# Kernel tuning notes

Measured on AMD Instinct MI355X. Metric: run time of the kernel, lower is better.

The kernel has to match this reference:

```python
import jax, jax.numpy as jnp
import numpy as np

B, S, D, H, E, K = 4, 512, 512, 2048, 8, 2
LN_EPS = 1e-5

def _ln(x, g, b):
    m = jnp.mean(x, axis=-1, keepdims=True)
    v = jnp.var(x, axis=-1, keepdims=True)
    return (x - m) / jnp.sqrt(v + LN_EPS) * g + b

def setup_inputs() -> dict:
    key = jax.random.key(0)
    ks = jax.random.split(key, 8)
    s = 0.02
    return {
        "x": jax.random.normal(ks[0], (B, S, D), dtype=jnp.float32),
        "context": jax.random.normal(ks[1], (B, S, D), dtype=jnp.float32),
        "quality": jax.random.uniform(ks[2], (B, 1), dtype=jnp.float32),
        "rn_g": jnp.ones((D,), jnp.float32), "rn_b": jnp.zeros((D,), jnp.float32),
        "cn_g": jnp.ones((D,), jnp.float32), "cn_b": jnp.zeros((D,), jnp.float32),
        "ctx_W": jax.random.normal(ks[3], (D, D), dtype=jnp.float32) * s,
        "ctx_b": jnp.zeros((D,), jnp.float32),
        "qual_W": jax.random.normal(ks[4], (1, D), dtype=jnp.float32) * s,
        "qual_b": jnp.zeros((D,), jnp.float32),
        "rtr_W": jax.random.normal(ks[5], (D, E), dtype=jnp.float32) * s,
        "rtr_b": jnp.zeros((E,), jnp.float32),
        "temperature": jnp.asarray(1.0, jnp.float32),
        "W1": jax.random.normal(ks[6], (E, D, H), dtype=jnp.float32) * s,
        "b1": jnp.zeros((E, H), jnp.float32),
        "W2": jax.random.normal(ks[7], (E, H, D), dtype=jnp.float32) * s,
        "b2": jnp.zeros((E, D), jnp.float32),
    }

def reference(x, context, quality, rn_g, rn_b, cn_g, cn_b, ctx_W, ctx_b,
              qual_W, qual_b, rtr_W, rtr_b, temperature, W1, b1, W2, b2):
    # router features: LN(x) + context_proj(LN(context)) + quality_proj(quality)
    rf = _ln(x, rn_g, rn_b) + (_ln(context, cn_g, cn_b) @ ctx_W + ctx_b)
    q = quality[:, None, :]                      # [B,1,1]
    rf = rf + (q @ qual_W + qual_b)              # broadcast [B,1,D] over seq
    logits = (rf @ rtr_W + rtr_b) / jnp.maximum(temperature, 0.25)  # [B,S,E]
    # eval mode: no router noise, no dropout
    topk_logits, topk_idx = jax.lax.top_k(logits, K)
    gates = jax.nn.softmax(topk_logits, axis=-1)                    # [B,S,K]
    # per-token per-expert combine weight (equivalent to masked dispatch)
    combine = jnp.sum(gates[..., None] * jax.nn.one_hot(topk_idx, E, dtype=x.dtype), axis=-2)  # [B,S,E]
    # dense all-expert FFN, combined with (mostly zero) gate weights
    h = jax.nn.gelu(jnp.einsum('bsd,edh->bseh', x, W1) + b1, approximate=False)  # [B,S,E,H]
    y = jnp.einsum('bseh,ehd->bsed', h, W2) + b2                                 # [B,S,E,D]
    out = jnp.einsum('bsed,bse->bsd', y, combine)
    # aux losses
    probs = jax.nn.softmax(logits, axis=-1)
    importance = probs.mean(axis=(0, 1))
    load_balance = jnp.mean((importance - 1.0 / E) ** 2)
    router_z = jnp.mean(jax.scipy.special.logsumexp(logits, axis=-1) ** 2)
    entropy = jnp.mean(-jnp.sum(probs * jnp.log(jnp.clip(probs, 1e-9, None)), axis=-1))
    aux = load_balance + 1e-3 * router_z - 1e-3 * entropy
    return out, load_balance, router_z, entropy, aux
```

## Files before the change

### kernel.cpp

```cpp
#include <hip/hip_runtime.h>
#include <hip/hip_bf16.h>
#include <math.h>

#define Bb 4
#define Ss 512
#define Dd 512
#define Hh 2048
#define Ee 8
#define TOKENS 2048
#define CAP 2048

typedef __attribute__((ext_vector_type(8))) _Float16 f16x8;
typedef __attribute__((ext_vector_type(4))) _Float16 f16x4;
typedef __attribute__((ext_vector_type(4))) float f32x4;

#define WS_CNT   0
#define WS_OFFS  32
#define WS_M1    128
#define WS_QV    16512
#define WS_CB    16544
#define WS_LIST  16640
#define WS_GLIST 82176
#define WS_LOG   147712
#define WS_XF    (WS_LOG + 65536)
#define WS_W1F   (WS_XF + 2097152)
#define WS_W2F   (WS_W1F + 16777216)
#define WS_HF    (WS_W2F + 16777216)

__device__ __forceinline__ float wred(float v) {
#pragma unroll
  for (int o = 32; o > 0; o >>= 1) v += __shfl_down(v, o);
  return v;
}

__device__ __forceinline__ float wredx(float v) {
#pragma unroll
  for (int o = 32; o > 0; o >>= 1) v += __shfl_xor(v, o);
  return v;
}

__device__ __forceinline__ float block_sum(float v, float* s4, int tid) {
  v = wred(v);
  __syncthreads();
  if ((tid & 63) == 0) s4[tid >> 6] = v;
  __syncthreads();
  return s4[0] + s4[1] + s4[2] + s4[3];
}

__device__ __forceinline__ float gelu_f(float v) {
  return 0.5f * v * (1.0f + erff(v * 0.7071067811865475f));
}

#define GL16(gp, lp) __builtin_amdgcn_global_load_lds( \
    (const __attribute__((address_space(1))) void*)(gp), \
    (__attribute__((address_space(3))) void*)(lp), 16, 0, 0)

__device__ __forceinline__ void convT_tile(const float* __restrict__ src,
    _Float16* __restrict__ dst, int R, int C, int bx, float* ls) {
  int nr = R >> 6, ncc = C >> 6;
  int e = bx / (nr * ncc);
  int rem = bx % (nr * ncc);
  int rt = rem / ncc, ct = rem % ncc;
  int tid = threadIdx.x;
  const float* s0 = src + (size_t)e * R * C + (size_t)(rt * 64) * C + ct * 64;
#pragma unroll
  for (int j = 0; j < 4; j++) {
    int li = j * 256 + tid;
    int rr = li >> 4, c4 = (li & 15) << 2;
    float4 v = *(const float4*)(s0 + (size_t)rr * C + c4);
    ls[rr * 65 + c4] = v.x;
    ls[rr * 65 + c4 + 1] = v.y;
    ls[rr * 65 + c4 + 2] = v.z;
    ls[rr * 65 + c4 + 3] = v.w;
  }
  __syncthreads();
#pragma unroll
  for (int j = 0; j < 4; j++) {
    int li = j * 256 + tid;
    int on = li >> 4, k4 = (li & 15) << 2;
    f16x4 o;
    o[0] = (_Float16)ls[(k4 + 0) * 65 + on];
    o[1] = (_Float16)ls[(k4 + 1) * 65 + on];
    o[2] = (_Float16)ls[(k4 + 2) * 65 + on];
    o[3] = (_Float16)ls[(k4 + 3) * 65 + on];
    *(f16x4*)(dst + ((size_t)e * C + ct * 64 + on) * R + rt * 64 + k4) = o;
  }
}

__global__ __launch_bounds__(256) void k_pre(
    const float* __restrict__ ctx_W, const float* __restrict__ rtr_W,
    const float* __restrict__ rtr_b, const float* __restrict__ qual_W,
    const float* __restrict__ qual_b, const float* __restrict__ ctx_b,
    const float* __restrict__ W1, const float* __restrict__ W2,
    float* __restrict__ M1, float* __restrict__ qv, float* __restrict__ cb,
    _Float16* __restrict__ w1f, _Float16* __restrict__ w2f) {
  __shared__ float ls[64 * 65];
  int bx = blockIdx.x;
  if (bx >= 513) {
    int cx = bx - 513;
    if (cx < Ee * 8 * 32) convT_tile(W1, w1f, Dd, Hh, cx, ls);
    else convT_tile(W2, w2f, Hh, Dd, cx - Ee * 8 * 32, ls);
    return;
  }
  int d = bx;
  int tid = threadIdx.x;
  if (tid >= 64) return;
  int lane = tid;
  if (d < Dd) {
    float acc[Ee] = {0.f, 0.f, 0.f, 0.f, 0.f, 0.f, 0.f, 0.f};
    for (int k = lane; k < Dd; k += 64) {
      float cw = ctx_W[d * Dd + k];
      const float* r = rtr_W + k * Ee;
#pragma unroll
      for (int e = 0; e < Ee; e++) acc[e] += cw * r[e];
    }
#pragma unroll
    for (int e = 0; e < Ee; e++) acc[e] = wred(acc[e]);
    if (lane == 0) {
#pragma unroll
      for (int e = 0; e < Ee; e++) M1[d * Ee + e] = acc[e];
    }
  } else {
    float aq[Ee] = {0.f, 0.f, 0.f, 0.f, 0.f, 0.f, 0.f, 0.f};
    float ab[Ee] = {0.f, 0.f, 0.f, 0.f, 0.f, 0.f, 0.f, 0.f};
    for (int k = lane; k < Dd; k += 64) {
      float qw = qual_W[k];
      float bb = ctx_b[k] + qual_b[k];
      const float* r = rtr_W + k * Ee;
#pragma unroll
      for (int e = 0; e < Ee; e++) {
        aq[e] += qw * r[e];
        ab[e] += bb * r[e];
      }
    }
#pragma unroll
    for (int e = 0; e < Ee; e++) {
      aq[e] = wred(aq[e]);
      ab[e] = wred(ab[e]);
    }
    if (lane == 0) {
#pragma unroll
      for (int e = 0; e < Ee; e++) {
        qv[e] = aq[e];
        cb[e] = ab[e] + rtr_b[e];
      }
    }
  }
}

__global__ __launch_bounds__(256) void k_logits(
    const float* __restrict__ x, const float* __restrict__ ctx,
    const float* __restrict__ quality, const float* __restrict__ rn_g,
    const float* __restrict__ rn_b, const float* __restrict__ cn_g,
    const float* __restrict__ cn_b, const float* __restrict__ rtr_W,
    const float* __restrict__ M1, const float* __restrict__ qv,
    const float* __restrict__ cb, const float* __restrict__ temperature,
    float* __restrict__ logitsS, _Float16* __restrict__ xf) {
  int wid = threadIdx.x >> 6, lane = threadIdx.x & 63;
  int t = blockIdx.x * 4 + wid;
  int d0 = lane * 8;

  float xv[8], cv[8];
  *(float4*)&xv[0] = *(const float4*)(x + (size_t)t * Dd + d0);
  *(float4*)&xv[4] = *(const float4*)(x + (size_t)t * Dd + d0 + 4);
  *(float4*)&cv[0] = *(const float4*)(ctx + (size_t)t * Dd + d0);
  *(float4*)&cv[4] = *(const float4*)(ctx + (size_t)t * Dd + d0 + 4);

  f16x8 xh;
#pragma unroll
  for (int d = 0; d < 8; d++) xh[d] = (_Float16)xv[d];
  *(f16x8*)(xf + (size_t)t * Dd + d0) = xh;

  float sx = 0.f, sc = 0.f;
#pragma unroll
  for (int d = 0; d < 8; d++) { sx += xv[d]; sc += cv[d]; }
  float mx = wredx(sx) * (1.f / Dd);
  float mc = wredx(sc) * (1.f / Dd);
  float vx = 0.f, vc = 0.f;
#pragma unroll
  for (int d = 0; d < 8; d++) {
    vx += (xv[d] - mx) * (xv[d] - mx);
    vc += (cv[d] - mc) * (cv[d] - mc);
  }
  float rsx = rsqrtf(wredx(vx) * (1.f / Dd) + 1e-5f);
  float rsc = rsqrtf(wredx(vc) * (1.f / Dd) + 1e-5f);

  float rg[8], rb[8], cg[8], cbb[8];
  *(float4*)&rg[0] = *(const float4*)(rn_g + d0);
  *(float4*)&rg[4] = *(const float4*)(rn_g + d0 + 4);
  *(float4*)&rb[0] = *(const float4*)(rn_b + d0);
  *(float4*)&rb[4] = *(const float4*)(rn_b + d0 + 4);
  *(float4*)&cg[0] = *(const float4*)(cn_g + d0);
  *(float4*)&cg[4] = *(const float4*)(cn_g + d0 + 4);
  *(float4*)&cbb[0] = *(const float4*)(cn_b + d0);
  *(float4*)&cbb[4] = *(const float4*)(cn_b + d0 + 4);

  float lg[Ee] = {0.f, 0.f, 0.f, 0.f, 0.f, 0.f, 0.f, 0.f};
#pragma unroll
  for (int d = 0; d < 8; d++) {
    float xn = (xv[d] - mx) * rsx * rg[d] + rb[d];
    float cn = (cv[d] - mc) * rsc * cg[d] + cbb[d];
    float rw[8], m1[8];
    *(float4*)&rw[0] = *(const float4*)(rtr_W + (size_t)(d0 + d) * Ee);
    *(float4*)&rw[4] = *(const float4*)(rtr_W + (size_t)(d0 + d) * Ee + 4);
    *(float4*)&m1[0] = *(const float4*)(M1 + (size_t)(d0 + d) * Ee);
    *(float4*)&m1[4] = *(const float4*)(M1 + (size_t)(d0 + d) * Ee + 4);
#pragma unroll
    for (int e = 0; e < Ee; e++) lg[e] += xn * rw[e] + cn * m1[e];
  }
#pragma unroll
  for (int e = 0; e < Ee; e++) lg[e] = wredx(lg[e]);

  if (lane == 0) {
    float invT = 1.f / fmaxf(temperature[0], 0.25f);
    float q = quality[t / Ss];
    float L[8];
#pragma unroll
    for (int e = 0; e < Ee; e++) L[e] = (lg[e] + q * qv[e] + cb[e]) * invT;
    *(float4*)(logitsS + (size_t)t * Ee) = *(float4*)&L[0];
    *(float4*)(logitsS + (size_t)t * Ee + 4) = *(float4*)&L[4];
  }
}

__global__ __launch_bounds__(256) void k_select(
    const float* __restrict__ logitsS, int* __restrict__ cnt,
    int* __restrict__ offs, int* __restrict__ list,
    float* __restrict__ glist, float* __restrict__ out) {
  __shared__ int scnt[Ee];
  __shared__ float s4[4];
  int tid = threadIdx.x;
  if (tid < Ee) scnt[tid] = 0;
  __syncthreads();

  float impL[Ee] = {0.f, 0.f, 0.f, 0.f, 0.f, 0.f, 0.f, 0.f};
  float zL = 0.f, eL = 0.f;

#pragma unroll
  for (int j = 0; j < 8; j++) {
    int t = j * 256 + tid;
    float L[8];
    *(float4*)&L[0] = *(const float4*)(logitsS + (size_t)t * Ee);
    *(float4*)&L[4] = *(const float4*)(logitsS + (size_t)t * Ee + 4);

    int i0 = 0;
#pragma unroll
    for (int e = 1; e < Ee; e++)
      if (L[e] > L[i0]) i0 = e;
    int i1 = (i0 == 0) ? 1 : 0;
#pragma unroll
    for (int e = 0; e < Ee; e++)
      if (e != i0 && L[e] > L[i1]) i1 = e;

    float e1 = __expf(L[i1] - L[i0]);
    float g0 = 1.f / (1.f + e1);
    float g1 = e1 / (1.f + e1);

    float m = L[i0];
    float p[8];
    float sum = 0.f;
#pragma unroll
    for (int e = 0; e < Ee; e++) {
      p[e] = __expf(L[e] - m);
      sum += p[e];
    }
    float lse = m + __logf(sum);
    float inv = 1.f / sum;
    zL += lse * lse;
#pragma unroll
    for (int e = 0; e < Ee; e++) {
      p[e] *= inv;
      eL -= p[e] * __logf(fmaxf(p[e], 1e-9f));
      impL[e] += p[e];
    }

    int s0 = atomicAdd(&scnt[i0], 1);
    list[i0 * CAP + s0] = t;
    glist[i0 * CAP + s0] = g0;
    int s1 = atomicAdd(&scnt[i1], 1);
    list[i1 * CAP + s1] = t;
    glist[i1 * CAP + s1] = g1;
  }

  float impS[Ee];
#pragma unroll
  for (int e = 0; e < Ee; e++) impS[e] = block_sum(impL[e], s4, tid);
  float zS = block_sum(zL, s4, tid);
  float eS = block_sum(eL, s4, tid);
  __syncthreads();

  if (tid == 0) {
    int s = 0;
#pragma unroll
    for (int e = 0; e < Ee; e++) {
      cnt[e] = scnt[e];
      offs[e] = s;
      s += scnt[e];
    }
    float lb = 0.f;
#pragma unroll
    for (int e = 0; e < Ee; e++) {
      float v = impS[e] * (1.f / TOKENS) - (1.f / Ee);
      lb += v * v;
    }
    lb *= (1.f / Ee);
    float rz = zS * (1.f / TOKENS);
    float en = eS * (1.f / TOKENS);
    float* sp = out + (size_t)Bb * Ss * Dd;
    sp[0] = lb;
    sp[1] = rz;
    sp[2] = en;
    sp[3] = lb + 0.001f * rz - 0.001f * en;
  }
}

__global__ __launch_bounds__(256) void k_mg1(
    const _Float16* __restrict__ xf, const _Float16* __restrict__ w1f,
    const float* __restrict__ b1,
    const int* __restrict__ cnt, const int* __restrict__ offs,
    const int* __restrict__ list, _Float16* __restrict__ hf) {
  int bx = blockIdx.x;
  int e = bx >> 8;
  int r = (bx >> 4) & 15;
  int c = bx & 15;
  int ne = cnt[e];
  if (r * 128 >= ne) return;
  int off = offs[e];

  __shared__ _Float16 As[8 * 128 * 8];
  __shared__ _Float16 Bs[8 * 128 * 8];
  __shared__ int stok[128];

  int tid = threadIdx.x;
  if (tid < 128) {
    int row = r * 128 + tid;
    stok[tid] = list[e * CAP + ((row < ne) ? row : (ne - 1))];
  }
  __syncthreads();

  size_t asrc[4], bsrc[4];
  int lq[4];
#pragma unroll
  for (int q = 0; q < 4; q++) {
    int idx = q * 256 + tid;
    int g = idx >> 7, row = idx & 127;
    asrc[q] = (size_t)stok[row] * Dd + g * 8;
    bsrc[q] = ((size_t)(e * Hh + c * 128 + row)) * Dd + g * 8;
    lq[q] = idx * 8;
  }

  int lane = tid & 63, wid = tid >> 6;
  int wm = wid >> 1, wn = wid & 1;
  int l15 = lane & 15, lg = lane >> 4;

  f32x4 acc[4][4] = {};

  for (int k0 = 0; k0 < Dd; k0 += 64) {
#pragma unroll
    for (int q = 0; q < 4; q++) {
      GL16(xf + asrc[q] + k0, &As[lq[q]]);
      GL16(w1f + bsrc[q] + k0, &Bs[lq[q]]);
    }
    __syncthreads();
    f16x8 a[2][4], b[2][4];
#pragma unroll
    for (int ks = 0; ks < 2; ks++) {
#pragma unroll
      for (int m = 0; m < 4; m++)
        a[ks][m] = *(const f16x8*)&As[(((ks * 4 + lg) << 7) + wm * 64 + m * 16 + l15) * 8];
#pragma unroll
      for (int n = 0; n < 4; n++)
        b[ks][n] = *(const f16x8*)&Bs[(((ks * 4 + lg) << 7) + wn * 64 + n * 16 + l15) * 8];
    }
#pragma unroll
    for (int ks = 0; ks < 2; ks++)
#pragma unroll
      for (int m = 0; m < 4; m++)
#pragma unroll
        for (int n = 0; n < 4; n++)
          acc[m][n] = __builtin_amdgcn_mfma_f32_16x16x32_f16(a[ks][m], b[ks][n], acc[m][n], 0, 0, 0);
    __syncthreads();
  }

  int lg4 = lg * 4;
#pragma unroll
  for (int n = 0; n < 4; n++) {
    int colg = c * 128 + wn * 64 + n * 16 + l15;
    float bias = b1[e * Hh + colg];
#pragma unroll
    for (int m = 0; m < 4; m++) {
#pragma unroll
      for (int j = 0; j < 4; j++) {
        int rowl = r * 128 + wm * 64 + m * 16 + lg4 + j;
        if (rowl < ne)
          hf[(size_t)(off + rowl) * Hh + colg] = (_Float16)gelu_f(acc[m][n][j] + bias);
      }
    }
  }
}

__global__ __launch_bounds__(256) void k_mg2(
    const _Float16* __restrict__ hf, const _Float16* __restrict__ w2f,
    const float* __restrict__ b2,
    const int* __restrict__ cnt, const int* __restrict__ offs,
    const int* __restrict__ list, const float* __restrict__ glist,
    float* __restrict__ out) {
  int bx = blockIdx.x;
  int e = bx >> 8;
  int r = (bx >> 4) & 15;
  int c = (bx >> 2) & 3;
  int kS = bx & 3;
  int ne = cnt[e];
  if (r * 128 >= ne) return;
  int off = offs[e];

  __shared__ _Float16 As[8 * 128 * 8];
  __shared__ _Float16 Bs[8 * 128 * 8];

  int tid = threadIdx.x;
  size_t kbase = (size_t)kS * 512;

  size_t asrc[4], bsrc[4];
  int lq[4];
#pragma unroll
  for (int q = 0; q < 4; q++) {
    int idx = q * 256 + tid;
    int g = idx >> 7, row = idx & 127;
    int ar = r * 128 + row;
    if (ar >= ne) ar = ne - 1;
    asrc[q] = (size_t)(off + ar) * Hh + kbase + g * 8;
    bsrc[q] = ((size_t)(e * Dd + c * 128 + row)) * Hh + kbase + g * 8;
    lq[q] = idx * 8;
  }

  int lane = tid & 63, wid = tid >> 6;
  int wm = wid >> 1, wn = wid & 1;
  int l15 = lane & 15, lg = lane >> 4;

  f32x4 acc[4][4] = {};

  for (int k0 = 0; k0 < 512; k0 += 64) {
#pragma unroll
    for (int q = 0; q < 4; q++) {
      GL16(hf + asrc[q] + k0, &As[lq[q]]);
      GL16(w2f + bsrc[q] + k0, &Bs[lq[q]]);
    }
    __syncthreads();
    f16x8 a[2][4], b[2][4];
#pragma unroll
    for (int ks = 0; ks < 2; ks++) {
#pragma unroll
      for (int m = 0; m < 4; m++)
        a[ks][m] = *(const f16x8*)&As[(((ks * 4 + lg) << 7) + wm * 64 + m * 16 + l15) * 8];
#pragma unroll
      for (int n = 0; n < 4; n++)
        b[ks][n] = *(const f16x8*)&Bs[(((ks * 4 + lg) << 7) + wn * 64 + n * 16 + l15) * 8];
    }
#pragma unroll
    for (int ks = 0; ks < 2; ks++)
#pragma unroll
      for (int m = 0; m < 4; m++)
#pragma unroll
        for (int n = 0; n < 4; n++)
          acc[m][n] = __builtin_amdgcn_mfma_f32_16x16x32_f16(a[ks][m], b[ks][n], acc[m][n], 0, 0, 0);
    __syncthreads();
  }

  int lg4 = lg * 4;
#pragma unroll
  for (int m = 0; m < 4; m++) {
#pragma unroll
    for (int j = 0; j < 4; j++) {
      int rowl = r * 128 + wm * 64 + m * 16 + lg4 + j;
      if (rowl < ne) {
        int tok = list[e * CAP + rowl];
        float gte = glist[e * CAP + rowl];
#pragma unroll
        for (int n = 0; n < 4; n++) {
          int colg = c * 128 + wn * 64 + n * 16 + l15;
          float v = acc[m][n][j] + (kS == 0 ? b2[e * Dd + colg] : 0.f);
          atomicAdd(&out[(size_t)tok * Dd + colg], gte * v);
        }
      }
    }
  }
}

extern "C" void kernel_launch(void* const* d_in, const int* in_sizes, int n_in,
                              void* d_out, int out_size, void* d_ws, size_t ws_size,
                              hipStream_t stream) {
  const float* x = (const float*)d_in[0];
  const float* ctx = (const float*)d_in[1];
  const float* quality = (const float*)d_in[2];
  const float* rn_g = (const float*)d_in[3];
  const float* rn_b = (const float*)d_in[4];
  const float* cn_g = (const float*)d_in[5];
  const float* cn_b = (const float*)d_in[6];
  const float* ctx_W = (const float*)d_in[7];
  const float* ctx_b = (const float*)d_in[8];
  const float* qual_W = (const float*)d_in[9];
  const float* qual_b = (const float*)d_in[10];
  const float* rtr_W = (const float*)d_in[11];
  const float* rtr_b = (const float*)d_in[12];
  const float* temperature = (const float*)d_in[13];
  const float* W1 = (const float*)d_in[14];
  const float* b1 = (const float*)d_in[15];
  const float* W2 = (const float*)d_in[16];
  const float* b2 = (const float*)d_in[17];
  float* out = (float*)d_out;

  char* w = (char*)d_ws;
  int* cnt = (int*)(w + WS_CNT);
  int* offs = (int*)(w + WS_OFFS);
  float* M1 = (float*)(w + WS_M1);
  float* qv = (float*)(w + WS_QV);
  float* cb = (float*)(w + WS_CB);
  int* list = (int*)(w + WS_LIST);
  float* glist = (float*)(w + WS_GLIST);
  float* logitsS = (float*)(w + WS_LOG);
  _Float16* xf = (_Float16*)(w + WS_XF);
  _Float16* w1f = (_Float16*)(w + WS_W1F);
  _Float16* w2f = (_Float16*)(w + WS_W2F);
  _Float16* hf = (_Float16*)(w + WS_HF);

  hipMemsetAsync(d_out, 0, (size_t)out_size * sizeof(float), stream);

  k_pre<<<513 + Ee * 8 * 32 * 2, 256, 0, stream>>>(
      ctx_W, rtr_W, rtr_b, qual_W, qual_b, ctx_b, W1, W2, M1, qv, cb, w1f, w2f);
  k_logits<<<TOKENS / 4, 256, 0, stream>>>(x, ctx, quality, rn_g, rn_b, cn_g, cn_b, rtr_W,
                                           M1, qv, cb, temperature, logitsS, xf);
  k_select<<<1, 256, 0, stream>>>(logitsS, cnt, offs, list, glist, out);
  k_mg1<<<Ee * 16 * 16, 256, 0, stream>>>(xf, w1f, b1, cnt, offs, list, hf);
  k_mg2<<<Ee * 16 * 4 * 4, 256, 0, stream>>>(hf, w2f, b2, cnt, offs, list, glist, out);
}
```

Before: 271.9 us.

## Double-buffer LDS tiles in expert GEMM kernels to overlap loads with MFMA

Both grouped expert GEMM kernels now keep two shared-memory buffers per operand. The next K-tile is issued into the spare buffer before the MFMAs run on the current one, with a single barrier per iteration. The aim is to hide global-to-LDS load latency behind compute. In exchange LDS use doubles to 64KB per block, which may lower occupancy. Correctness also depends on whether the GL16 async loads are waited on properly before the barrier.

```diff
diff --git a/kernel.cpp b/kernel.cpp
--- a/kernel.cpp
+++ b/kernel.cpp
@@ -326,8 +326,8 @@
   if (r * 128 >= ne) return;
   int off = offs[e];
 
-  __shared__ _Float16 As[8 * 128 * 8];
-  __shared__ _Float16 Bs[8 * 128 * 8];
+  __shared__ _Float16 As[2][8 * 128 * 8];
+  __shared__ _Float16 Bs[2][8 * 128 * 8];
   __shared__ int stok[128];
 
   int tid = threadIdx.x;
@@ -354,31 +354,39 @@
 
   f32x4 acc[4][4] = {};
 
+#pragma unroll
+  for (int q = 0; q < 4; q++) {
+    GL16(xf + asrc[q], &As[0][lq[q]]);
+    GL16(w1f + bsrc[q], &Bs[0][lq[q]]);
+  }
+  __syncthreads();
+
+  int cur = 0;
   for (int k0 = 0; k0 < Dd; k0 += 64) {
-#pragma unroll
-    for (int q = 0; q < 4; q++) {
-      GL16(xf + asrc[q] + k0, &As[lq[q]]);
-      GL16(w1f + bsrc[q] + k0, &Bs[lq[q]]);
+    if (k0 + 64 < Dd) {
+#pragma unroll
+      for (int q = 0; q < 4; q++) {
+        GL16(xf + asrc[q] + k0 + 64, &As[cur ^ 1][lq[q]]);
+        GL16(w1f + bsrc[q] + k0 + 64, &Bs[cur ^ 1][lq[q]]);
+      }
+    }
+#pragma unroll
+    for (int ks = 0; ks < 2; ks++) {
+      f16x8 a[4], b[4];
+#pragma unroll
+      for (int m = 0; m < 4; m++)
+        a[m] = *(const f16x8*)&As[cur][(((ks * 4 + lg) << 7) + wm * 64 + m * 16 + l15) * 8];
+#pragma unroll
+      for (int n = 0; n < 4; n++)
+        b[n] = *(const f16x8*)&Bs[cur][(((ks * 4 + lg) << 7) + wn * 64 + n * 16 + l15) * 8];
+#pragma unroll
+      for (int m = 0; m < 4; m++)
+#pragma unroll
+        for (int n = 0; n < 4; n++)
+          acc[m][n] = __builtin_amdgcn_mfma_f32_16x16x32_f16(a[m], b[n], acc[m][n], 0, 0, 0);
     }
     __syncthreads();
-    f16x8 a[2][4], b[2][4];
-#pragma unroll
-    for (int ks = 0; ks < 2; ks++) {
-#pragma unroll
-      for (int m = 0; m < 4; m++)
-        a[ks][m] = *(const f16x8*)&As[(((ks * 4 + lg) << 7) + wm * 64 + m * 16 + l15) * 8];
-#pragma unroll
-      for (int n = 0; n < 4; n++)
-        b[ks][n] = *(const f16x8*)&Bs[(((ks * 4 + lg) << 7) + wn * 64 + n * 16 + l15) * 8];
-    }
-#pragma unroll
-    for (int ks = 0; ks < 2; ks++)
-#pragma unroll
-      for (int m = 0; m < 4; m++)
-#pragma unroll
-        for (int n = 0; n < 4; n++)
-          acc[m][n] = __builtin_amdgcn_mfma_f32_16x16x32_f16(a[ks][m], b[ks][n], acc[m][n], 0, 0, 0);
-    __syncthreads();
+    cur ^= 1;
   }
 
   int lg4 = lg * 4;
@@ -413,8 +421,8 @@
   if (r * 128 >= ne) return;
   int off = offs[e];
 
-  __shared__ _Float16 As[8 * 128 * 8];
-  __shared__ _Float16 Bs[8 * 128 * 8];
+  __shared__ _Float16 As[2][8 * 128 * 8];
+  __shared__ _Float16 Bs[2][8 * 128 * 8];
 
   int tid = threadIdx.x;
   size_t kbase = (size_t)kS * 512;
@@ -438,31 +446,39 @@
 
   f32x4 acc[4][4] = {};
 
+#pragma unroll
+  for (int q = 0; q < 4; q++) {
+    GL16(hf + asrc[q], &As[0][lq[q]]);
+    GL16(w2f + bsrc[q], &Bs[0][lq[q]]);
+  }
+  __syncthreads();
+
+  int cur = 0;
   for (int k0 = 0; k0 < 512; k0 += 64) {
-#pragma unroll
-    for (int q = 0; q < 4; q++) {
-      GL16(hf + asrc[q] + k0, &As[lq[q]]);
-      GL16(w2f + bsrc[q] + k0, &Bs[lq[q]]);
+    if (k0 + 64 < 512) {
+#pragma unroll
+      for (int q = 0; q < 4; q++) {
+        GL16(hf + asrc[q] + k0 + 64, &As[cur ^ 1][lq[q]]);
+        GL16(w2f + bsrc[q] + k0 + 64, &Bs[cur ^ 1][lq[q]]);
+      }
+    }
+#pragma unroll
+    for (int ks = 0; ks < 2; ks++) {
+      f16x8 a[4], b[4];
+#pragma unroll
+      for (int m = 0; m < 4; m++)
+        a[m] = *(const f16x8*)&As[cur][(((ks * 4 + lg) << 7) + wm * 64 + m * 16 + l15) * 8];
+#pragma unroll
+      for (int n = 0; n < 4; n++)
+        b[n] = *(const f16x8*)&Bs[cur][(((ks * 4 + lg) << 7) + wn * 64 + n * 16 + l15) * 8];
+#pragma unroll
+      for (int m = 0; m < 4; m++)
+#pragma unroll
+        for (int n = 0; n < 4; n++)
+          acc[m][n] = __builtin_amdgcn_mfma_f32_16x16x32_f16(a[m], b[n], acc[m][n], 0, 0, 0);
     }
     __syncthreads();
-    f16x8 a[2][4], b[2][4];
-#pragma unroll
-    for (int ks = 0; ks < 2; ks++) {
-#pragma unroll
-      for (int m = 0; m < 4; m++)
-        a[ks][m] = *(const f16x8*)&As[(((ks * 4 + lg) << 7) + wm * 64 + m * 16 + l15) * 8];
-#pragma unroll
-      for (int n = 0; n < 4; n++)
-        b[ks][n] = *(const f16x8*)&Bs[(((ks * 4 + lg) << 7) + wn * 64 + n * 16 + l15) * 8];
-    }
-#pragma unroll
-    for (int ks = 0; ks < 2; ks++)
-#pragma unroll
-      for (int m = 0; m < 4; m++)
-#pragma unroll
-        for (int n = 0; n < 4; n++)
-          acc[m][n] = __builtin_amdgcn_mfma_f32_16x16x32_f16(a[ks][m], b[ks][n], acc[m][n], 0, 0, 0);
-    __syncthreads();
+    cur ^= 1;
   }
 
   int lg4 = lg * 4;
```

After: 300.4 us. 1.11x slower.

## Replace atomic scatter in second expert GEMM with buffered partials and combine kernel

Applied to the files above, without the earlier changes.

The second expert GEMM now writes its split-K partial results as fp16 into a per-split buffer instead of atomically adding gated values into the output. A new combine kernel gathers, for each token, its two expert slots across the four K splits. It adds bias, applies gates and writes the output directly, which also removes the output memset. This trades float atomics for extra global traffic, an additional launch, and fp16 rounding of the partial sums.

```diff
diff --git a/kernel.cpp b/kernel.cpp
--- a/kernel.cpp
+++ b/kernel.cpp
@@ -26,6 +26,8 @@
 #define WS_W1F   (WS_XF + 2097152)
 #define WS_W2F   (WS_W1F + 16777216)
 #define WS_HF    (WS_W2F + 16777216)
+#define WS_YB    (WS_HF + 16777216)
+#define WS_SEL   (WS_YB + 16777216)
 
 __device__ __forceinline__ float wred(float v) {
 #pragma unroll
@@ -225,7 +227,8 @@
 __global__ __launch_bounds__(256) void k_select(
     const float* __restrict__ logitsS, int* __restrict__ cnt,
     int* __restrict__ offs, int* __restrict__ list,
-    float* __restrict__ glist, float* __restrict__ out) {
+    float* __restrict__ glist, int* __restrict__ sel,
+    float* __restrict__ out) {
   __shared__ int scnt[Ee];
   __shared__ float s4[4];
   int tid = threadIdx.x;
@@ -276,9 +279,11 @@
     int s0 = atomicAdd(&scnt[i0], 1);
     list[i0 * CAP + s0] = t;
     glist[i0 * CAP + s0] = g0;
+    sel[t * 2 + 0] = (i0 << 12) | s0;
     int s1 = atomicAdd(&scnt[i1], 1);
     list[i1 * CAP + s1] = t;
     glist[i1 * CAP + s1] = g1;
+    sel[t * 2 + 1] = (i1 << 12) | s1;
   }
 
   float impS[Ee];
@@ -400,10 +405,8 @@
 
 __global__ __launch_bounds__(256) void k_mg2(
     const _Float16* __restrict__ hf, const _Float16* __restrict__ w2f,
-    const float* __restrict__ b2,
     const int* __restrict__ cnt, const int* __restrict__ offs,
-    const int* __restrict__ list, const float* __restrict__ glist,
-    float* __restrict__ out) {
+    _Float16* __restrict__ yb) {
   int bx = blockIdx.x;
   int e = bx >> 8;
   int r = (bx >> 4) & 15;
@@ -472,17 +475,49 @@
     for (int j = 0; j < 4; j++) {
       int rowl = r * 128 + wm * 64 + m * 16 + lg4 + j;
       if (rowl < ne) {
-        int tok = list[e * CAP + rowl];
-        float gte = glist[e * CAP + rowl];
+        _Float16* yp = yb + ((size_t)kS * 4096 + off + rowl) * Dd;
 #pragma unroll
         for (int n = 0; n < 4; n++) {
           int colg = c * 128 + wn * 64 + n * 16 + l15;
-          float v = acc[m][n][j] + (kS == 0 ? b2[e * Dd + colg] : 0.f);
-          atomicAdd(&out[(size_t)tok * Dd + colg], gte * v);
+          yp[colg] = (_Float16)acc[m][n][j];
         }
       }
     }
   }
+}
+
+__global__ __launch_bounds__(256) void k_comb(
+    const _Float16* __restrict__ yb, const int* __restrict__ sel,
+    const float* __restrict__ glist, const int* __restrict__ offs,
+    const float* __restrict__ b2, float* __restrict__ out) {
+  int t = blockIdx.x * 4 + (threadIdx.x >> 6);
+  int lane = threadIdx.x & 63;
+  int c0 = lane * 8;
+
+  float acc[8] = {0.f, 0.f, 0.f, 0.f, 0.f, 0.f, 0.f, 0.f};
+#pragma unroll
+  for (int k = 0; k < 2; k++) {
+    int pk = sel[t * 2 + k];
+    int e = pk >> 12, pos = pk & 4095;
+    int slot = offs[e] + pos;
+    float g = glist[e * CAP + pos];
+    float pa[8] = {0.f, 0.f, 0.f, 0.f, 0.f, 0.f, 0.f, 0.f};
+#pragma unroll
+    for (int s = 0; s < 4; s++) {
+      f16x8 v = *(const f16x8*)(yb + ((size_t)s * 4096 + slot) * Dd + c0);
+#pragma unroll
+      for (int j = 0; j < 8; j++) pa[j] += (float)v[j];
+    }
+    const float* bb = b2 + e * Dd + c0;
+    float b4[8];
+    *(float4*)&b4[0] = *(const float4*)bb;
+    *(float4*)&b4[4] = *(const float4*)(bb + 4);
+#pragma unroll
+    for (int j = 0; j < 8; j++) acc[j] += g * (pa[j] + b4[j]);
+  }
+  float* op = out + (size_t)t * Dd + c0;
+  *(float4*)op = *(float4*)&acc[0];
+  *(float4*)(op + 4) = *(float4*)&acc[4];
 }
 
 extern "C" void kernel_launch(void* const* d_in, const int* in_sizes, int n_in,
@@ -521,14 +556,15 @@
   _Float16* w1f = (_Float16*)(w + WS_W1F);
   _Float16* w2f = (_Float16*)(w + WS_W2F);
   _Float16* hf = (_Float16*)(w + WS_HF);
-
-  hipMemsetAsync(d_out, 0, (size_t)out_size * sizeof(float), stream);
+  _Float16* yb = (_Float16*)(w + WS_YB);
+  int* sel = (int*)(w + WS_SEL);
 
   k_pre<<<513 + Ee * 8 * 32 * 2, 256, 0, stream>>>(
       ctx_W, rtr_W, rtr_b, qual_W, qual_b, ctx_b, W1, W2, M1, qv, cb, w1f, w2f);
   k_logits<<<TOKENS / 4, 256, 0, stream>>>(x, ctx, quality, rn_g, rn_b, cn_g, cn_b, rtr_W,
                                            M1, qv, cb, temperature, logitsS, xf);
-  k_select<<<1, 256, 0, stream>>>(logitsS, cnt, offs, list, glist, out);
+  k_select<<<1, 256, 0, stream>>>(logitsS, cnt, offs, list, glist, sel, out);
   k_mg1<<<Ee * 16 * 16, 256, 0, stream>>>(xf, w1f, b1, cnt, offs, list, hf);
-  k_mg2<<<Ee * 16 * 4 * 4, 256, 0, stream>>>(hf, w2f, b2, cnt, offs, list, glist, out);
-}
+  k_mg2<<<Ee * 16 * 4 * 4, 256, 0, stream>>>(hf, w2f, cnt, offs, yb);
+  k_comb<<<TOKENS / 4, 256, 0, stream>>>(yb, sel, glist, offs, b2, out);
+}
```

Result: faster. 256.7 us (-5.6%).
